# Performance work log

Hardware: AMD Instinct MI355X
Metric: run time of the kernel (lower is better)

The kernel has to match this reference:

```python
import jax, jax.numpy as jnp
import numpy as np

N, D, H, HD, R, K, TM = 32768, 128, 2, 64, 2, 32, 2
E_EDGES, M_MOTIFS, NG = 262144, 131072, 32
EPS = 1e-5
BETA_MAX = 5.0
GRAD_CLIP = 1.0
STATE_CLIP = 10.0
DAMPING = 1.0

def _isp(x):
    # inverse softplus of init values (params stored pre-softplus)
    return float(np.log(np.expm1(x)))

LAM2_RAW, LAM3_RAW, LAMM_RAW = _isp(1.0), _isp(0.5), _isp(1.0)
B2_RAW, B3_RAW, BM_RAW = _isp(1.0), _isp(1.0), _isp(1.0)


def layernorm(x, g, b):
    mu = x.mean(-1, keepdims=True)
    v = ((x - mu) ** 2).mean(-1, keepdims=True)
    return g * (x - mu) * jax.lax.rsqrt(v + EPS) + b


def seg_lse(s, seg, n, beta):
    # tempered logsumexp over segments: (1/beta) log sum_j exp(beta*s_j); s:[items,H] -> [n,H]
    sb = beta * s
    m = jax.ops.segment_max(sb, seg, num_segments=n)
    m = jnp.where(jnp.isfinite(m), m, 0.0)
    z = jax.ops.segment_sum(jnp.exp(sb - m[seg]), seg, num_segments=n)
    return jnp.where(z > 0, (m + jnp.log(jnp.maximum(z, 1e-30))) / beta, 0.0)


def energy(X, a_2, ln_gamma, ln_beta, W_Q2, W_K2, W_Q3, W_K3, T_tau, W_Qm, W_Km, B_mem,
           c_2, u_2, c_3, u_3, v_3, t_tau, batch):
    sp = jax.nn.softplus
    lam2, lam3, lamm = sp(LAM2_RAW), sp(LAM3_RAW), sp(LAMM_RAW)
    b2 = jnp.minimum(sp(B2_RAW), BETA_MAX)
    b3 = jnp.minimum(sp(B3_RAW), BETA_MAX)
    bm = jnp.minimum(sp(BM_RAW), BETA_MAX)
    G = layernorm(X, ln_gamma, ln_beta)
    # pairwise Q2/K2 term over edges (c_2 <- u_2) with learned per-edge bias a_2
    Q2 = jnp.einsum('nd,hzd->nhz', G, W_Q2)  # [N,H,HD]
    K2 = jnp.einsum('nd,hzd->nhz', G, W_K2)
    s2 = jnp.einsum('ehz,ehz->eh', Q2[c_2], K2[u_2]) / np.sqrt(HD) + a_2  # [E,H]
    e_pair = -lam2 * seg_lse(s2, c_2, N, b2).sum(-1)  # [N]
    # rank-R bilinear motif term over (c_3,u_3,v_3) with type embedding T_tau
    Q3 = jnp.einsum('nd,hzd->nhz', G, W_Q3).reshape(N, H, R, HD)
    K3 = jnp.einsum('nd,hzd->nhz', G, W_K3).reshape(N, H, R, HD)
    qk = jnp.einsum('mhrz,mhrz->mhr', Q3[c_3], K3[u_3])
    tv = jnp.einsum('mhrz,mhrz->mhr', T_tau[t_tau], K3[v_3])
    s3 = (qk * tv).sum(-1) / HD  # [M,H]
    e_motif = -lam3 * seg_lse(s3, c_3, N, b3).sum(-1)
    # K-slot memory term
    Qm = jnp.einsum('nd,hzd->nhz', G, W_Qm)
    Km = jnp.einsum('kd,hzd->hkz', B_mem, W_Km)
    sm = jnp.einsum('nhz,hkz->nhk', Qm, Km) / np.sqrt(HD)
    e_mem = -(lamm / bm) * jax.nn.logsumexp(bm * sm, axis=-1).sum(-1)
    e_node = 0.5 * (X * X).sum(-1) + e_pair + e_motif + e_mem
    return jax.ops.segment_sum(e_node, batch, num_segments=NG)  # per-graph energy [NG]


def setup_inputs() -> dict:
    key = jax.random.key(0)
    ks = jax.random.split(key, 16)
    inp = {}
    inp['X'] = jax.random.normal(ks[0], (N, D), jnp.float32)
    inp['c_2'] = jax.random.randint(ks[1], (E_EDGES,), 0, N)
    inp['u_2'] = jax.random.randint(ks[2], (E_EDGES,), 0, N)
    inp['c_3'] = jax.random.randint(ks[3], (M_MOTIFS,), 0, N)
    inp['u_3'] = jax.random.randint(ks[4], (M_MOTIFS,), 0, N)
    inp['v_3'] = jax.random.randint(ks[5], (M_MOTIFS,), 0, N)
    inp['t_tau'] = jax.random.randint(ks[6], (M_MOTIFS,), 0, TM)
    inp['batch'] = jnp.sort(jax.random.randint(ks[7], (N,), 0, NG))
    inp['a_2'] = 0.1 * jax.random.normal(ks[8], (E_EDGES, H), jnp.float32)
    inp['step_size'] = jnp.full((1,), 0.1, jnp.float32)
    inp['ln_gamma'] = jnp.ones((D,), jnp.float32)
    inp['ln_beta'] = jnp.zeros((D,), jnp.float32)
    s = 1.0 / np.sqrt(D)
    inp['W_Q2'] = s * jax.random.normal(ks[9], (H, HD, D), jnp.float32)
    inp['W_K2'] = s * jax.random.normal(ks[10], (H, HD, D), jnp.float32)
    inp['W_Q3'] = 0.5 * s * jax.random.normal(ks[11], (H, R * HD, D), jnp.float32)
    inp['W_K3'] = 0.5 * s * jax.random.normal(ks[12], (H, R * HD, D), jnp.float32)
    inp['T_tau'] = 0.02 * jax.random.normal(ks[13], (TM, H, R, HD), jnp.float32)
    inp['W_Qm'] = 0.5 * s * jax.random.normal(ks[14], (H, HD, D), jnp.float32)
    inp['W_Km'] = 0.5 * s * jax.random.normal(ks[15], (H, HD, D), jnp.float32)
    inp['B_mem'] = s * jax.random.normal(jax.random.fold_in(key, 99), (K, D), jnp.float32)
    return inp


def reference(X, c_2, u_2, c_3, u_3, v_3, t_tau, batch, a_2, step_size,
              ln_gamma, ln_beta, W_Q2, W_K2, W_Q3, W_K3, T_tau, W_Qm, W_Km, B_mem):
    Eg, vjp = jax.vjp(
        lambda Xv: energy(Xv, a_2, ln_gamma, ln_beta, W_Q2, W_K2, W_Q3, W_K3, T_tau,
                          W_Qm, W_Km, B_mem, c_2, u_2, c_3, u_3, v_3, t_tau, batch), X)
    gX, = vjp(jnp.ones_like(Eg))
    gnorm = jnp.linalg.norm(gX, axis=-1, keepdims=True)
    gX = gX * (GRAD_CLIP / jnp.maximum(gnorm, GRAD_CLIP))
    X_next = X - step_size[0] * DAMPING * gX
    snorm = jnp.linalg.norm(X_next, axis=-1, keepdims=True)
    X_next = X_next * (STATE_CLIP / jnp.maximum(snorm, STATE_CLIP))
    return X_next, Eg
```

## Files before the change

kernel.cpp:

```cpp
#include <hip/hip_runtime.h>
#include <hip/hip_bf16.h>
#include <math.h>

typedef __hip_bfloat16 bf16;
typedef short bf16x8 __attribute__((ext_vector_type(8)));
typedef float f32x4 __attribute__((ext_vector_type(4)));

#define N_NODES 32768
#define D_DIM 128
#define E_EDG 262144
#define M_MOT 131072
#define NG_G 32
#define F_TOT 832

__device__ __forceinline__ int pidx(int n){ return ((n & 7) << 12) | (n >> 3); }

__device__ __forceinline__ float wsum64(float v){
#pragma unroll
  for (int o = 32; o > 0; o >>= 1) v += __shfl_xor(v, o, 64);
  return v;
}
__device__ __forceinline__ float hsum32(float v){
#pragma unroll
  for (int o = 16; o > 0; o >>= 1) v += __shfl_xor(v, o, 64);
  return v;
}
__device__ __forceinline__ float hmax32(float v){
#pragma unroll
  for (int o = 16; o > 0; o >>= 1) v = fmaxf(v, __shfl_xor(v, o, 64));
  return v;
}
__device__ __forceinline__ float hsum8(float v){
#pragma unroll
  for (int o = 4; o > 0; o >>= 1) v += __shfl_xor(v, o, 64);
  return v;
}
__device__ __forceinline__ float bflo(unsigned u){ return __uint_as_float(u << 16); }
__device__ __forceinline__ float bfhi(unsigned u){ return __uint_as_float(u & 0xffff0000u); }
__device__ __forceinline__ unsigned packbf(float x, float y){
  bf16 a = __float2bfloat16(x), b = __float2bfloat16(y);
  unsigned short ua = *(unsigned short*)&a, ub = *(unsigned short*)&b;
  return (unsigned)ua | ((unsigned)ub << 16);
}
__device__ __forceinline__ void unpk8(uint4 p, float* f){
  f[0] = bflo(p.x); f[1] = bfhi(p.x); f[2] = bflo(p.y); f[3] = bfhi(p.y);
  f[4] = bflo(p.z); f[5] = bfhi(p.z); f[6] = bflo(p.w); f[7] = bfhi(p.w);
}

__global__ __launch_bounds__(256) void k_phaseA(
    const int* c2, const int* u2, const int* c3, const int* u3, const int* v3,
    const float* wq2, const float* wk2, const float* wq3, const float* wk3,
    const float* wqm, const float* wkm, const float* bmem, const float* Ttau,
    int* cnt, float* Wcat, bf16* Ttb, float* Mprod){
  __shared__ float KmL[64];
  int b = blockIdx.x, t = threadIdx.x;
  if (b < 1024){
    int* base = cnt + (size_t)(b & 7) * 5 * N_NODES;
    int i = b * 256 + t;
    atomicAdd(&base[pidx(c2[i])], 1);
    atomicAdd(&base[N_NODES + pidx(u2[i])], 1);
    if (i < M_MOT){
      atomicAdd(&base[2 * N_NODES + pidx(c3[i])], 1);
      atomicAdd(&base[3 * N_NODES + pidx(u3[i])], 1);
      atomicAdd(&base[4 * N_NODES + pidx(v3[i])], 1);
    }
  } else if (b < 1440){
    int idx = (b - 1024) * 256 + t;
    if (idx < 768 * D_DIM){
      int f = idx / D_DIM, d = idx - f * D_DIM;
      const float* src; int fr;
      if      (f < 128){ src = wq2; fr = f; }
      else if (f < 256){ src = wk2; fr = f - 128; }
      else if (f < 512){ src = wq3; fr = f - 256; }
      else             { src = wk3; fr = f - 512; }
      Wcat[f * D_DIM + d] = src[fr * D_DIM + d];
    } else {
      int j = idx - 768 * D_DIM;
      Ttb[j] = __float2bfloat16(Ttau[j]);
    }
  } else {
    int hk = b - 1440;
    int h = hk >> 5, k = hk & 31;
    if (t < 64){
      const float* wrow = wkm + (size_t)(h * 64 + t) * D_DIM;
      const float* brow = bmem + k * D_DIM;
      float acc = 0.f;
      for (int d = 0; d < D_DIM; d++) acc += wrow[d] * brow[d];
      KmL[t] = acc;
    }
    __syncthreads();
    if (t < 128){
      const float* w = wqm + (size_t)(h * 64) * 128 + t;
      float acc = 0.f;
      for (int z = 0; z < 64; z++) acc += w[z * 128] * KmL[z];
      Mprod[t * 64 + hk] = acc;
    }
  }
}

__global__ __launch_bounds__(1024) void k_phaseB(
    int* cntcur, int* off,
    const float* X, const float* gamma, const float* beta,
    bf16* Gb, float* mu, float* rstd, float* e_node,
    const float* Wcat, const float* Mprod, bf16* wfF, bf16* wfB){
  __shared__ int sd[1024];
  int b = blockIdx.x, t = threadIdx.x;
  if (b < 5){
    int a = b;
    int* cbase = cntcur + a * N_NODES;
    int* o = off + a * (N_NODES + 1);
    int loc[32];
    int sum = 0;
#pragma unroll
    for (int j = 0; j < 32; j++){
      int idx = t * 32 + j;
      int tot = 0;
#pragma unroll
      for (int rr = 0; rr < 8; rr++) tot += cbase[(size_t)rr * 5 * N_NODES + idx];
      loc[j] = sum; sum += tot;
    }
    sd[t] = sum;
    __syncthreads();
    for (int s = 1; s < 1024; s <<= 1){
      int v = (t >= s) ? sd[t - s] : 0;
      __syncthreads();
      sd[t] += v;
      __syncthreads();
    }
    int excl = sd[t] - sum;
#pragma unroll
    for (int j = 0; j < 32; j++){
      int val = excl + loc[j];
      o[t * 32 + j] = val;
      cbase[t * 32 + j] = val;
    }
    if (t == 1023) o[N_NODES] = sd[1023];
  } else if (b < 2053){
    int wv = t >> 6, l = t & 63;
    int n = (b - 5) * 16 + wv;
    float2 x2 = ((const float2*)(X + (size_t)n * 128))[l];
    float sumx = wsum64(x2.x + x2.y);
    float sumxx = wsum64(x2.x * x2.x + x2.y * x2.y);
    float m = sumx * (1.0f / 128.0f);
    float var = sumxx * (1.0f / 128.0f) - m * m;
    float rs = rsqrtf(var + 1e-5f);
    float2 gg = ((const float2*)gamma)[l];
    float2 bb = ((const float2*)beta)[l];
    ((unsigned*)(Gb + (size_t)n * 128))[l] =
        packbf(gg.x * (x2.x - m) * rs + bb.x, gg.y * (x2.y - m) * rs + bb.y);
    if (l == 0){ mu[n] = m; rstd[n] = rs; e_node[n] = 0.5f * sumxx; }
  } else {
    int idx = (b - 2053) * 1024 + t;
    int j = idx & 7, lane = (idx >> 3) & 63, tt = idx >> 9;
    {
      int tn = tt >> 2, kt = tt & 3;
      int f = tn * 16 + (lane & 15), d = kt * 32 + (lane >> 4) * 8 + j;
      float v = (f < 768) ? Wcat[f * 128 + d] : 0.125f * Mprod[d * 64 + (f - 768)];
      wfF[idx] = __float2bfloat16(v);
    }
    {
      int td = tt / 26, tf = tt - td * 26;
      int f = tf * 32 + (lane >> 4) * 8 + j, d = td * 16 + (lane & 15);
      float v = (f < 768) ? Wcat[f * 128 + d] : -0.125f * Mprod[d * 64 + (f - 768)];
      wfB[idx] = __float2bfloat16(v);
    }
  }
}

__global__ __launch_bounds__(256) void k_phaseC(
    const bf16* Gb, const bf16* wfF, bf16* P,
    const int* c2, const int* u2, const int* c3, const int* u3, const int* v3,
    const int* t3, int* cur,
    uint2* lec, uint2* leu, uint2* lmc, uint2* lmu, uint2* lmv){
  int b = blockIdx.x;
  int g = b / 29, r = b - g * 29;
  if (r < 13){
    __shared__ unsigned shP[64 * 36];
    int f = g * 13 + r;
    int bx = f & 511, by = f >> 9;
    int wave = threadIdx.x >> 6, lane = threadIdx.x & 63;
    int m0 = bx * 64 + wave * 16;
    int tn0 = by * 4;
    int rw = lane & 15, quad = lane >> 4;
    const bf16* aptr = Gb + (size_t)(m0 + rw) * 128 + quad * 8;
    bf16x8 a[4];
#pragma unroll
    for (int kt = 0; kt < 4; kt++) a[kt] = *(const bf16x8*)(aptr + kt * 32);
    f32x4 acc[4];
#pragma unroll
    for (int i = 0; i < 4; i++) acc[i] = (f32x4){0.f, 0.f, 0.f, 0.f};
#pragma unroll
    for (int nf = 0; nf < 4; nf++){
      int tn = tn0 + nf;
#pragma unroll
      for (int kt = 0; kt < 4; kt++){
        bf16x8 bb = *(const bf16x8*)(wfF + (((size_t)tn * 4 + kt) * 64 + lane) * 8);
        acc[nf] = __builtin_amdgcn_mfma_f32_16x16x32_bf16(bb, a[kt], acc[nf], 0, 0, 0);
      }
    }
    int lrow = wave * 16 + rw;
#pragma unroll
    for (int nf = 0; nf < 4; nf++){
      unsigned lo = packbf(acc[nf][0], acc[nf][1]);
      unsigned hi = packbf(acc[nf][2], acc[nf][3]);
      *(uint2*)&shP[lrow * 36 + nf * 8 + quad * 2] = make_uint2(lo, hi);
    }
    __syncthreads();
    int t = threadIdx.x;
    int orow = t >> 2, s = t & 3;
    uint4 v0 = *(const uint4*)&shP[orow * 36 + s * 4];
    uint4 v1 = *(const uint4*)&shP[orow * 36 + 16 + s * 4];
    uint4* prow = (uint4*)(P + (size_t)(bx * 64 + orow) * F_TOT) + tn0 * 2 + s;
    prow[0] = v0;
    prow[4] = v1;
  } else {
    int j = g * 16 + (r - 13);
    int range = j >> 3;
    int res = b & 7;
    int i = range * 256 + threadIdx.x;
    {
      int c = c2[i], u = u2[i];
      if ((c & 7) == res){
        int pos = atomicAdd(&cur[pidx(c)], 1);
        lec[pos] = make_uint2((unsigned)u, (unsigned)i);
      }
      if ((u & 7) == res){
        int pos = atomicAdd(&cur[N_NODES + pidx(u)], 1);
        leu[pos] = make_uint2((unsigned)c, (unsigned)i);
      }
    }
    if (i < M_MOT){
      int c = c3[i], u = u3[i], v = v3[i], mt = t3[i];
      if ((c & 7) == res){
        int pos = atomicAdd(&cur[2 * N_NODES + pidx(c)], 1);
        lmc[pos] = make_uint2((unsigned)(u | (v << 16)), (unsigned)(mt | (i << 5)));
      }
      if ((u & 7) == res){
        int pos = atomicAdd(&cur[3 * N_NODES + pidx(u)], 1);
        lmu[pos] = make_uint2((unsigned)c, (unsigned)i);
      }
      if ((v & 7) == res){
        int pos = atomicAdd(&cur[4 * N_NODES + pidx(v)], 1);
        lmv[pos] = make_uint2((unsigned)(c | (mt << 16)), (unsigned)i);
      }
    }
  }
}

__global__ __launch_bounds__(256) void k_fused_c(const bf16* P, const uint2* lec, const uint2* lmc,
                   const bf16* Ttb, const float* a2, const int* off_ec, const int* off_mc,
                   float* s2, float* rz2, float* s3, float* qkb, float* tvb, float* rz3,
                   bf16* dP, float* e_pair, float* e_mot, float* e_mem){
  int b = blockIdx.x;
  int type = b % 3, grp = b / 3;
  int wave = threadIdx.x >> 6, z = threadIdx.x & 63;
  int n = grp * 4 + wave;
  int l = z & 31, lh = z >> 5;
  int pn = pidx(n);

  if (type == 0){
    int q = z >> 4, l16 = z & 15, hg = l16 >> 3;
    int beg = off_ec[pn], end = off_ec[pn + 1];
    uint4 qp = ((const uint4*)(P + (size_t)n * F_TOT))[l16];
    float qv[8]; unpk8(qp, qv);
    float acc[8] = {0,0,0,0,0,0,0,0};
    float zz = 0.f;
    int iters = (end - beg + 3) >> 2;
    for (int it = 0; it < iters; it++){
      int idx = beg + 4 * it + q;
      bool valid = idx < end;
      int idc = valid ? idx : end - 1;
      uint2 pl = lec[idc];
      float2 av = *(const float2*)(a2 + (size_t)pl.y * 2);
      uint4 kp = ((const uint4*)(P + (size_t)pl.x * F_TOT + 128))[l16];
      float kv[8]; unpk8(kp, kv);
      float d = 0.f;
#pragma unroll
      for (int j = 0; j < 8; j++) d += qv[j] * kv[j];
      float s = hsum8(d) * 0.125f + (hg ? av.y : av.x);
      if (valid && (l16 & 7) == 0) s2[2 * pl.y + hg] = s;
      float ex = valid ? expf(s) : 0.f;
#pragma unroll
      for (int j = 0; j < 8; j++) acc[j] += ex * kv[j];
      zz += ex;
    }
#pragma unroll
    for (int j = 0; j < 8; j++){
      acc[j] += __shfl_xor(acc[j], 16, 64);
      acc[j] += __shfl_xor(acc[j], 32, 64);
    }
    zz += __shfl_xor(zz, 16, 64);
    zz += __shfl_xor(zz, 32, 64);
    float rz = (zz > 0.f) ? 1.0f / zz : 0.f;
    float coef = -0.125f * rz;
    if (z < 16){
      uint4 o;
      o.x = packbf(coef * acc[0], coef * acc[1]);
      o.y = packbf(coef * acc[2], coef * acc[3]);
      o.z = packbf(coef * acc[4], coef * acc[5]);
      o.w = packbf(coef * acc[6], coef * acc[7]);
      ((uint4*)(dP + (size_t)n * F_TOT))[l16] = o;
      if ((l16 & 7) == 0) rz2[n * 2 + hg] = rz;
    }
    float eterm = (zz > 0.f) ? -logf(zz) : 0.f;
    float eo = __shfl(eterm, 8, 64);
    if (z == 0) e_pair[n] = eterm + eo;
  } else if (type == 1){
    int g = l >> 3, hg = g >> 1;
    int beg = off_mc[pn], end = off_mc[pn + 1];
    uint4 qp = ((const uint4*)(P + (size_t)n * F_TOT + 256))[l];
    float qv[8]; unpk8(qp, qv);
    float acc[8] = {0,0,0,0,0,0,0,0};
    float zz = 0.f;
    int iters = (end - beg + 1) >> 1;
    for (int it = 0; it < iters; it++){
      int idx = beg + 2 * it + lh;
      bool valid = idx < end;
      int idc = valid ? idx : end - 1;
      uint2 pl = lmc[idc];
      int u = pl.x & 0xffff, v = pl.x >> 16;
      int tix = pl.y & 31; unsigned m = pl.y >> 5;
      uint4 kup = ((const uint4*)(P + (size_t)u * F_TOT + 512))[l];
      uint4 kvp = ((const uint4*)(P + (size_t)v * F_TOT + 512))[l];
      uint4 tp  = ((const uint4*)(Ttb + (size_t)tix * 256))[l];
      float k[8], vv[8], pt[8];
      unpk8(kup, k); unpk8(kvp, vv); unpk8(tp, pt);
      float dq = 0.f, dt = 0.f;
#pragma unroll
      for (int j = 0; j < 8; j++){ dq += qv[j] * k[j]; dt += pt[j] * vv[j]; }
      float qk = hsum8(dq);
      float tv = hsum8(dt);
      if (valid && (l & 7) == 0){ qkb[(size_t)4 * m + g] = qk; tvb[(size_t)4 * m + g] = tv; }
      float w = qk * tv;
      float s = (w + __shfl_xor(w, 8, 64)) * (1.0f / 64.0f);
      if (valid && (l & 15) == 0) s3[2 * m + hg] = s;
      float ex = valid ? expf(s) : 0.f;
      float et = ex * tv;
#pragma unroll
      for (int j = 0; j < 8; j++) acc[j] += et * k[j];
      zz += ex;
    }
#pragma unroll
    for (int j = 0; j < 8; j++) acc[j] += __shfl_xor(acc[j], 32, 64);
    zz += __shfl_xor(zz, 32, 64);
    float rz = (zz > 0.f) ? 1.0f / zz : 0.f;
    float coef = (-0.5f / 64.0f) * rz;
    if (z < 32){
      uint4 o;
      o.x = packbf(coef * acc[0], coef * acc[1]);
      o.y = packbf(coef * acc[2], coef * acc[3]);
      o.z = packbf(coef * acc[4], coef * acc[5]);
      o.w = packbf(coef * acc[6], coef * acc[7]);
      ((uint4*)(dP + (size_t)n * F_TOT + 256))[l] = o;
      if ((l & 15) == 0) rz3[n * 2 + hg] = rz;
    }
    float eterm = (zz > 0.f) ? -0.5f * logf(zz) : 0.f;
    float eo = __shfl(eterm, 16, 64);
    if (z == 0) e_mot[n] = eterm + eo;
  } else {
    unsigned short us = ((const unsigned short*)(P + (size_t)n * F_TOT + 768))[z];
    float s = __uint_as_float((unsigned)us << 16);
    float mx = hmax32(s);
    float ex = expf(s - mx);
    float se = hsum32(ex);
    float p = ex / se;
    bf16 pb = __float2bfloat16(p);
    ((unsigned short*)(dP + (size_t)n * F_TOT + 768))[z] = *(unsigned short*)&pb;
    float eterm = -(mx + logf(se));
    float eo = __shfl(eterm, z ^ 32, 64);
    if (z == 0) e_mem[n] = eterm + eo;
  }
}

__global__ __launch_bounds__(256) void k_phaseE(const bf16* P, const uint2* leu,
                    const uint2* lmu, const uint2* lmv, const bf16* Ttb,
                    const float* s2, const float* rz2, const float* s3, const float* rz3,
                    const float* qkb, const float* tvb,
                    const int* off_eu, const int* off_mu, const int* off_mv, bf16* dP,
                    const float* e_node, const float* e_pair, const float* e_mot,
                    const float* e_mem, const int* batch, float* Eg){
  __shared__ float eg[NG_G];
  int b = blockIdx.x;
  if (b < 128){
    int t = threadIdx.x;
    if (t < NG_G) eg[t] = 0.f;
    __syncthreads();
    int n = b * 256 + t;
    float e = e_node[n] + e_pair[n] + e_mot[n] + e_mem[n];
    atomicAdd(&eg[batch[n]], e);
    __syncthreads();
    if (t < NG_G) atomicAdd(&Eg[t], eg[t]);
    return;
  }
  int b2 = b - 128;
  int type = b2 & 1, grp = b2 >> 1;
  int wave = threadIdx.x >> 6, z = threadIdx.x & 63;
  int n = grp * 4 + wave;
  int pn = pidx(n);

  if (type == 0){
    int e8 = z >> 3, l8 = z & 7;
    int beg = off_eu[pn], end = off_eu[pn + 1];
    float acc[16];
#pragma unroll
    for (int j = 0; j < 16; j++) acc[j] = 0.f;
    int iters = (end - beg + 7) >> 3;
    for (int it = 0; it < iters; it++){
      int idx = beg + 8 * it + e8;
      bool valid = idx < end;
      int idc = valid ? idx : end - 1;
      uint2 pl = leu[idc];
      const uint4* qrow = (const uint4*)(P + (size_t)pl.x * F_TOT);
      uint4 qp0 = qrow[l8];
      uint4 qp1 = qrow[l8 + 8];
      float2 sv = *(const float2*)(s2 + 2 * (size_t)pl.y);
      float2 rv = *(const float2*)(rz2 + 2 * (size_t)pl.x);
      float qv0[8], qv1[8];
      unpk8(qp0, qv0); unpk8(qp1, qv1);
      float p0 = valid ? expf(sv.x) * rv.x : 0.f;
      float p1 = valid ? expf(sv.y) * rv.y : 0.f;
#pragma unroll
      for (int j = 0; j < 8; j++){
        acc[j]     += p0 * qv0[j];
        acc[8 + j] += p1 * qv1[j];
      }
    }
#pragma unroll
    for (int j = 0; j < 16; j++){
      acc[j] += __shfl_xor(acc[j], 8, 64);
      acc[j] += __shfl_xor(acc[j], 16, 64);
      acc[j] += __shfl_xor(acc[j], 32, 64);
    }
    if (z < 8){
      uint4 o0, o1;
      o0.x = packbf(-0.125f * acc[0], -0.125f * acc[1]);
      o0.y = packbf(-0.125f * acc[2], -0.125f * acc[3]);
      o0.z = packbf(-0.125f * acc[4], -0.125f * acc[5]);
      o0.w = packbf(-0.125f * acc[6], -0.125f * acc[7]);
      o1.x = packbf(-0.125f * acc[8], -0.125f * acc[9]);
      o1.y = packbf(-0.125f * acc[10], -0.125f * acc[11]);
      o1.z = packbf(-0.125f * acc[12], -0.125f * acc[13]);
      o1.w = packbf(-0.125f * acc[14], -0.125f * acc[15]);
      uint4* dst = (uint4*)(dP + (size_t)n * F_TOT + 128);
      dst[z] = o0;
      dst[z + 8] = o1;
    }
  } else {
    int m4 = z >> 4, l16 = z & 15;
    int g0 = l16 >> 3;
    float acc[16];
#pragma unroll
    for (int j = 0; j < 16; j++) acc[j] = 0.f;
    {
      int beg = off_mu[pn], end = off_mu[pn + 1];
      int iters = (end - beg + 3) >> 2;
      for (int it = 0; it < iters; it++){
        int idx = beg + 4 * it + m4;
        bool valid = idx < end;
        int idc = valid ? idx : end - 1;
        uint2 pl = lmu[idc];
        const uint4* qrow = (const uint4*)(P + (size_t)pl.x * F_TOT + 256);
        uint4 qp0 = qrow[l16];
        uint4 qp1 = qrow[l16 + 16];
        float2 sv = *(const float2*)(s3 + 2 * (size_t)pl.y);
        float2 rv = *(const float2*)(rz3 + 2 * (size_t)pl.x);
        float4 tq = *(const float4*)(tvb + 4 * (size_t)pl.y);
        float t0 = g0 ? tq.y : tq.x;
        float t1 = g0 ? tq.w : tq.z;
        float qv0[8], qv1[8];
        unpk8(qp0, qv0); unpk8(qp1, qv1);
        float w0 = valid ? expf(sv.x) * rv.x * t0 : 0.f;
        float w1 = valid ? expf(sv.y) * rv.y * t1 : 0.f;
#pragma unroll
        for (int j = 0; j < 8; j++){
          acc[j]     += w0 * qv0[j];
          acc[8 + j] += w1 * qv1[j];
        }
      }
    }
    {
      int beg = off_mv[pn], end = off_mv[pn + 1];
      int iters = (end - beg + 3) >> 2;
      for (int it = 0; it < iters; it++){
        int idx = beg + 4 * it + m4;
        bool valid = idx < end;
        int idc = valid ? idx : end - 1;
        uint2 pl = lmv[idc];
        unsigned c = pl.x & 0xffff, tix = pl.x >> 16;
        const uint4* trow = (const uint4*)(Ttb + (size_t)tix * 256);
        uint4 tp0 = trow[l16];
        uint4 tp1 = trow[l16 + 16];
        float2 sv = *(const float2*)(s3 + 2 * (size_t)pl.y);
        float2 rv = *(const float2*)(rz3 + 2 * (size_t)c);
        float4 qq = *(const float4*)(qkb + 4 * (size_t)pl.y);
        float q0 = g0 ? qq.y : qq.x;
        float q1 = g0 ? qq.w : qq.z;
        float pt0[8], pt1[8];
        unpk8(tp0, pt0); unpk8(tp1, pt1);
        float w0 = valid ? expf(sv.x) * rv.x * q0 : 0.f;
        float w1 = valid ? expf(sv.y) * rv.y * q1 : 0.f;
#pragma unroll
        for (int j = 0; j < 8; j++){
          acc[j]     += w0 * pt0[j];
          acc[8 + j] += w1 * pt1[j];
        }
      }
    }
#pragma unroll
    for (int j = 0; j < 16; j++){
      acc[j] += __shfl_xor(acc[j], 16, 64);
      acc[j] += __shfl_xor(acc[j], 32, 64);
    }
    const float cst = -0.5f / 64.0f;
    if (z < 16){
      uint4 o0, o1;
      o0.x = packbf(cst * acc[0], cst * acc[1]);
      o0.y = packbf(cst * acc[2], cst * acc[3]);
      o0.z = packbf(cst * acc[4], cst * acc[5]);
      o0.w = packbf(cst * acc[6], cst * acc[7]);
      o1.x = packbf(cst * acc[8], cst * acc[9]);
      o1.y = packbf(cst * acc[10], cst * acc[11]);
      o1.z = packbf(cst * acc[12], cst * acc[13]);
      o1.w = packbf(cst * acc[14], cst * acc[15]);
      uint4* dst = (uint4*)(dP + (size_t)n * F_TOT + 512);
      dst[l16] = o0;
      dst[l16 + 16] = o1;
    }
  }
}

__global__ __launch_bounds__(256) void k_bwd_mfma(const bf16* dP, const bf16* wfB, float* dG){
  int wave = threadIdx.x >> 6, lane = threadIdx.x & 63;
  int m0 = blockIdx.x * 64 + wave * 16;
  int rw = lane & 15, quad = lane >> 4;
  const bf16* aptr = dP + (size_t)(m0 + rw) * F_TOT + quad * 8;
  f32x4 acc[8];
#pragma unroll
  for (int i = 0; i < 8; i++) acc[i] = (f32x4){0.f, 0.f, 0.f, 0.f};
  for (int kt = 0; kt < 26; kt++){
    bf16x8 a = *(const bf16x8*)(aptr + kt * 32);
#pragma unroll
    for (int td = 0; td < 8; td++){
      bf16x8 b = *(const bf16x8*)(wfB + (((size_t)td * 26 + kt) * 64 + lane) * 8);
      acc[td] = __builtin_amdgcn_mfma_f32_16x16x32_bf16(a, b, acc[td], 0, 0, 0);
    }
  }
#pragma unroll
  for (int td = 0; td < 8; td++){
    int col = td * 16 + rw;
#pragma unroll
    for (int r = 0; r < 4; r++){
      int row = m0 + quad * 4 + r;
      dG[(size_t)row * 128 + col] = acc[td][r];
    }
  }
}

__global__ __launch_bounds__(256) void k_finalize(const float* X, const float* dG, const float* gamma,
                    const float* mu, const float* rstd, const float* step_p,
                    const float* Eg, float* out){
  int wave = threadIdx.x >> 6, l = threadIdx.x & 63;
  int n = blockIdx.x * 4 + wave;
  float2 x2 = ((const float2*)(X + (size_t)n * 128))[l];
  float2 dg2 = ((const float2*)(dG + (size_t)n * 128))[l];
  float2 gg = ((const float2*)gamma)[l];
  float rs = rstd[n], m = mu[n];
  float xh0 = (x2.x - m) * rs, xh1 = (x2.y - m) * rs;
  float dxh0 = dg2.x * gg.x, dxh1 = dg2.y * gg.y;
  float s1 = wsum64(dxh0 + dxh1);
  float s2v = wsum64(dxh0 * xh0 + dxh1 * xh1);
  float g0 = x2.x + rs * (dxh0 - s1 * (1.0f / 128) - xh0 * (s2v * (1.0f / 128)));
  float g1 = x2.y + rs * (dxh1 - s1 * (1.0f / 128) - xh1 * (s2v * (1.0f / 128)));
  float gn = sqrtf(wsum64(g0 * g0 + g1 * g1));
  float gc = 1.0f / fmaxf(gn, 1.0f);
  g0 *= gc; g1 *= gc;
  float step = step_p[0];
  float xn0 = x2.x - step * g0, xn1 = x2.y - step * g1;
  float sn = sqrtf(wsum64(xn0 * xn0 + xn1 * xn1));
  float sc = 10.0f / fmaxf(sn, 10.0f);
  ((float2*)(out + (size_t)n * 128))[l] = make_float2(xn0 * sc, xn1 * sc);
  if (blockIdx.x == 0 && threadIdx.x < NG_G)
    out[(size_t)N_NODES * 128 + threadIdx.x] = Eg[threadIdx.x];
}

extern "C" void kernel_launch(void* const* d_in, const int* in_sizes, int n_in,
                              void* d_out, int out_size, void* d_ws, size_t ws_size,
                              hipStream_t stream) {
  const float* X     = (const float*)d_in[0];
  const int*  c_2    = (const int*) d_in[1];
  const int*  u_2    = (const int*) d_in[2];
  const int*  c_3    = (const int*) d_in[3];
  const int*  u_3    = (const int*) d_in[4];
  const int*  v_3    = (const int*) d_in[5];
  const int*  t_tau  = (const int*) d_in[6];
  const int*  batch  = (const int*) d_in[7];
  const float* a_2   = (const float*)d_in[8];
  const float* step_s= (const float*)d_in[9];
  const float* ln_g  = (const float*)d_in[10];
  const float* ln_b  = (const float*)d_in[11];
  const float* W_Q2  = (const float*)d_in[12];
  const float* W_K2  = (const float*)d_in[13];
  const float* W_Q3  = (const float*)d_in[14];
  const float* W_K3  = (const float*)d_in[15];
  const float* T_tau = (const float*)d_in[16];
  const float* W_Qm  = (const float*)d_in[17];
  const float* W_Km  = (const float*)d_in[18];
  const float* B_mem = (const float*)d_in[19];
  float* out = (float*)d_out;

  char* wb = (char*)d_ws;
  float* Wcat   = (float*)wb; wb += 768 * D_DIM * 4;
  float* Mprod  = (float*)wb; wb += 8192 * 4;
  float* mu     = (float*)wb; wb += N_NODES * 4;
  float* rstd   = (float*)wb; wb += N_NODES * 4;
  float* s2     = (float*)wb; wb += (size_t)E_EDG * 2 * 4;
  float* rz2    = (float*)wb; wb += N_NODES * 2 * 4;
  float* s3     = (float*)wb; wb += (size_t)M_MOT * 2 * 4;
  float* qkb    = (float*)wb; wb += (size_t)M_MOT * 4 * 4;
  float* tvb    = (float*)wb; wb += (size_t)M_MOT * 4 * 4;
  float* rz3    = (float*)wb; wb += N_NODES * 2 * 4;
  float* e_node = (float*)wb; wb += N_NODES * 4;
  float* e_pair = (float*)wb; wb += N_NODES * 4;
  float* e_mot  = (float*)wb; wb += N_NODES * 4;
  float* e_mem  = (float*)wb; wb += N_NODES * 4;
  float* Eg     = (float*)wb; wb += NG_G * 4;
  float* dG     = (float*)wb; wb += (size_t)N_NODES * D_DIM * 4;
  bf16* Gb      = (bf16*)wb;  wb += (size_t)N_NODES * D_DIM * 2;
  bf16* P       = (bf16*)wb;  wb += (size_t)N_NODES * F_TOT * 2;
  bf16* dP      = (bf16*)wb;  wb += (size_t)N_NODES * F_TOT * 2;
  bf16* wfF     = (bf16*)wb;  wb += 106496 * 2;
  bf16* wfB     = (bf16*)wb;  wb += 106496 * 2;
  bf16* Ttb     = (bf16*)wb;  wb += 8192 * 2;
  int* cntcur   = (int*)wb;   wb += 8 * 5 * N_NODES * 4;
  int* off      = (int*)wb;   wb += 5 * (N_NODES + 1) * 4;
  wb = (char*)(((size_t)wb + 15) & ~(size_t)15);
  uint2* lec    = (uint2*)wb; wb += (size_t)E_EDG * 8;
  uint2* leu    = (uint2*)wb; wb += (size_t)E_EDG * 8;
  uint2* lmc    = (uint2*)wb; wb += (size_t)M_MOT * 8;
  uint2* lmu    = (uint2*)wb; wb += (size_t)M_MOT * 8;
  uint2* lmv    = (uint2*)wb; wb += (size_t)M_MOT * 8;

  const int* off_ec = off;
  const int* off_eu = off + (N_NODES + 1);
  const int* off_mc = off + 2 * (N_NODES + 1);
  const int* off_mu = off + 3 * (N_NODES + 1);
  const int* off_mv = off + 4 * (N_NODES + 1);

  hipMemsetAsync(cntcur, 0, (size_t)8 * 5 * N_NODES * sizeof(int), stream);
  hipMemsetAsync(Eg, 0, NG_G * sizeof(float), stream);
  hipLaunchKernelGGL(k_phaseA, dim3(1504), dim3(256), 0, stream,
                     c_2, u_2, c_3, u_3, v_3, W_Q2, W_K2, W_Q3, W_K3,
                     W_Qm, W_Km, B_mem, T_tau, cntcur, Wcat, Ttb, Mprod);
  hipLaunchKernelGGL(k_phaseB, dim3(2157), dim3(1024), 0, stream,
                     cntcur, off, X, ln_g, ln_b, Gb, mu, rstd, e_node,
                     Wcat, Mprod, wfF, wfB);
  hipLaunchKernelGGL(k_phaseC, dim3(512 * 29), dim3(256), 0, stream,
                     Gb, wfF, P, c_2, u_2, c_3, u_3, v_3, t_tau, cntcur,
                     lec, leu, lmc, lmu, lmv);
  hipLaunchKernelGGL(k_fused_c, dim3(3 * (N_NODES / 4)), dim3(256), 0, stream,
                     P, lec, lmc, Ttb, a_2, off_ec, off_mc,
                     s2, rz2, s3, qkb, tvb, rz3, dP, e_pair, e_mot, e_mem);
  hipLaunchKernelGGL(k_phaseE, dim3(128 + 2 * (N_NODES / 4)), dim3(256), 0, stream,
                     P, leu, lmu, lmv, Ttb, s2, rz2, s3, rz3, qkb, tvb,
                     off_eu, off_mu, off_mv, dP,
                     e_node, e_pair, e_mot, e_mem, batch, Eg);
  hipLaunchKernelGGL(k_bwd_mfma, dim3(N_NODES / 64), dim3(256), 0, stream, dP, wfB, dG);
  hipLaunchKernelGGL(k_finalize, dim3(N_NODES / 4), dim3(256), 0, stream,
                     X, dG, ln_g, mu, rstd, step_s, Eg, out);
}
```

Before: 401.9 us.

## Parallelize count reduction in separate kernel; process more edges per wave in fused gather

Moves the summation of eight replicated per-node counters out of the five-block scan in phaseB into a new wide kernel, so the scan blocks only read one vectorized count array. In k_fused_c, the pair and motif loops now have each lane handle both heads (8 lanes per edge, 16 per motif), so each wave iteration covers twice as many edges/motifs with wider per-lane loads and fewer shuffles per item. This costs an extra kernel launch and more registers per thread in the fused kernel.

```diff
diff --git a/kernel.cpp b/kernel.cpp
--- a/kernel.cpp
+++ b/kernel.cpp
@@ -98,6 +98,18 @@
   }
 }
 
+__global__ __launch_bounds__(256) void k_reduce8(int* cnt){
+  int idx = blockIdx.x * 256 + threadIdx.x;
+  int4* base = (int4*)cnt;
+  int4 s = base[idx];
+#pragma unroll
+  for (int rr = 1; rr < 8; rr++){
+    int4 v = *(const int4*)(cnt + (size_t)rr * 5 * N_NODES + 4 * (size_t)idx);
+    s.x += v.x; s.y += v.y; s.z += v.z; s.w += v.w;
+  }
+  base[idx] = s;
+}
+
 __global__ __launch_bounds__(1024) void k_phaseB(
     int* cntcur, int* off,
     const float* X, const float* gamma, const float* beta,
@@ -106,19 +118,17 @@
   __shared__ int sd[1024];
   int b = blockIdx.x, t = threadIdx.x;
   if (b < 5){
-    int a = b;
-    int* cbase = cntcur + a * N_NODES;
-    int* o = off + a * (N_NODES + 1);
+    int* c = cntcur + b * N_NODES;
+    int* o = off + b * (N_NODES + 1);
+    int4 lv[8];
+    const int4* c4 = (const int4*)c;
+#pragma unroll
+    for (int j4 = 0; j4 < 8; j4++) lv[j4] = c4[t * 8 + j4];
+    int* lvp = (int*)lv;
     int loc[32];
     int sum = 0;
 #pragma unroll
-    for (int j = 0; j < 32; j++){
-      int idx = t * 32 + j;
-      int tot = 0;
-#pragma unroll
-      for (int rr = 0; rr < 8; rr++) tot += cbase[(size_t)rr * 5 * N_NODES + idx];
-      loc[j] = sum; sum += tot;
-    }
+    for (int j = 0; j < 32; j++){ loc[j] = sum; sum += lvp[j]; }
     sd[t] = sum;
     __syncthreads();
     for (int s = 1; s < 1024; s <<= 1){
@@ -132,7 +142,7 @@
     for (int j = 0; j < 32; j++){
       int val = excl + loc[j];
       o[t * 32 + j] = val;
-      cbase[t * 32 + j] = val;
+      c[t * 32 + j] = val;
     }
     if (t == 1023) o[N_NODES] = sd[1023];
   } else if (b < 2053){
@@ -255,108 +265,154 @@
   int type = b % 3, grp = b / 3;
   int wave = threadIdx.x >> 6, z = threadIdx.x & 63;
   int n = grp * 4 + wave;
-  int l = z & 31, lh = z >> 5;
   int pn = pidx(n);
 
   if (type == 0){
-    int q = z >> 4, l16 = z & 15, hg = l16 >> 3;
+    int e8 = z >> 3, l8 = z & 7;
     int beg = off_ec[pn], end = off_ec[pn + 1];
-    uint4 qp = ((const uint4*)(P + (size_t)n * F_TOT))[l16];
-    float qv[8]; unpk8(qp, qv);
-    float acc[8] = {0,0,0,0,0,0,0,0};
-    float zz = 0.f;
-    int iters = (end - beg + 3) >> 2;
+    const uint4* qrow = (const uint4*)(P + (size_t)n * F_TOT);
+    uint4 qp0 = qrow[l8], qp1 = qrow[l8 + 8];
+    float qv0[8], qv1[8]; unpk8(qp0, qv0); unpk8(qp1, qv1);
+    float acc0[8] = {0,0,0,0,0,0,0,0}, acc1[8] = {0,0,0,0,0,0,0,0};
+    float zz0 = 0.f, zz1 = 0.f;
+    int iters = (end - beg + 7) >> 3;
     for (int it = 0; it < iters; it++){
-      int idx = beg + 4 * it + q;
+      int idx = beg + 8 * it + e8;
       bool valid = idx < end;
       int idc = valid ? idx : end - 1;
       uint2 pl = lec[idc];
       float2 av = *(const float2*)(a2 + (size_t)pl.y * 2);
-      uint4 kp = ((const uint4*)(P + (size_t)pl.x * F_TOT + 128))[l16];
-      float kv[8]; unpk8(kp, kv);
-      float d = 0.f;
-#pragma unroll
-      for (int j = 0; j < 8; j++) d += qv[j] * kv[j];
-      float s = hsum8(d) * 0.125f + (hg ? av.y : av.x);
-      if (valid && (l16 & 7) == 0) s2[2 * pl.y + hg] = s;
-      float ex = valid ? expf(s) : 0.f;
-#pragma unroll
-      for (int j = 0; j < 8; j++) acc[j] += ex * kv[j];
-      zz += ex;
+      const uint4* krow = (const uint4*)(P + (size_t)pl.x * F_TOT + 128);
+      uint4 kp0 = krow[l8], kp1 = krow[l8 + 8];
+      float kv0[8], kv1[8]; unpk8(kp0, kv0); unpk8(kp1, kv1);
+      float d0 = 0.f, d1 = 0.f;
+#pragma unroll
+      for (int j = 0; j < 8; j++){ d0 += qv0[j] * kv0[j]; d1 += qv1[j] * kv1[j]; }
+      float s0 = hsum8(d0) * 0.125f + av.x;
+      float s1 = hsum8(d1) * 0.125f + av.y;
+      if (valid && l8 == 0) *(float2*)(s2 + 2 * (size_t)pl.y) = make_float2(s0, s1);
+      float ex0 = valid ? expf(s0) : 0.f;
+      float ex1 = valid ? expf(s1) : 0.f;
+#pragma unroll
+      for (int j = 0; j < 8; j++){ acc0[j] += ex0 * kv0[j]; acc1[j] += ex1 * kv1[j]; }
+      zz0 += ex0; zz1 += ex1;
     }
 #pragma unroll
     for (int j = 0; j < 8; j++){
-      acc[j] += __shfl_xor(acc[j], 16, 64);
-      acc[j] += __shfl_xor(acc[j], 32, 64);
-    }
-    zz += __shfl_xor(zz, 16, 64);
-    zz += __shfl_xor(zz, 32, 64);
-    float rz = (zz > 0.f) ? 1.0f / zz : 0.f;
-    float coef = -0.125f * rz;
-    if (z < 16){
-      uint4 o;
-      o.x = packbf(coef * acc[0], coef * acc[1]);
-      o.y = packbf(coef * acc[2], coef * acc[3]);
-      o.z = packbf(coef * acc[4], coef * acc[5]);
-      o.w = packbf(coef * acc[6], coef * acc[7]);
-      ((uint4*)(dP + (size_t)n * F_TOT))[l16] = o;
-      if ((l16 & 7) == 0) rz2[n * 2 + hg] = rz;
-    }
-    float eterm = (zz > 0.f) ? -logf(zz) : 0.f;
-    float eo = __shfl(eterm, 8, 64);
-    if (z == 0) e_pair[n] = eterm + eo;
+      acc0[j] += __shfl_xor(acc0[j], 8, 64);
+      acc0[j] += __shfl_xor(acc0[j], 16, 64);
+      acc0[j] += __shfl_xor(acc0[j], 32, 64);
+      acc1[j] += __shfl_xor(acc1[j], 8, 64);
+      acc1[j] += __shfl_xor(acc1[j], 16, 64);
+      acc1[j] += __shfl_xor(acc1[j], 32, 64);
+    }
+    zz0 += __shfl_xor(zz0, 8, 64); zz0 += __shfl_xor(zz0, 16, 64); zz0 += __shfl_xor(zz0, 32, 64);
+    zz1 += __shfl_xor(zz1, 8, 64); zz1 += __shfl_xor(zz1, 16, 64); zz1 += __shfl_xor(zz1, 32, 64);
+    float rz0 = (zz0 > 0.f) ? 1.0f / zz0 : 0.f;
+    float rz1 = (zz1 > 0.f) ? 1.0f / zz1 : 0.f;
+    float c0 = -0.125f * rz0, c1 = -0.125f * rz1;
+    if (z < 8){
+      uint4 o0, o1;
+      o0.x = packbf(c0 * acc0[0], c0 * acc0[1]);
+      o0.y = packbf(c0 * acc0[2], c0 * acc0[3]);
+      o0.z = packbf(c0 * acc0[4], c0 * acc0[5]);
+      o0.w = packbf(c0 * acc0[6], c0 * acc0[7]);
+      o1.x = packbf(c1 * acc1[0], c1 * acc1[1]);
+      o1.y = packbf(c1 * acc1[2], c1 * acc1[3]);
+      o1.z = packbf(c1 * acc1[4], c1 * acc1[5]);
+      o1.w = packbf(c1 * acc1[6], c1 * acc1[7]);
+      uint4* dst = (uint4*)(dP + (size_t)n * F_TOT);
+      dst[z] = o0;
+      dst[z + 8] = o1;
+    }
+    if (z == 0){
+      *(float2*)(rz2 + 2 * (size_t)n) = make_float2(rz0, rz1);
+      float e0 = (zz0 > 0.f) ? -logf(zz0) : 0.f;
+      float e1 = (zz1 > 0.f) ? -logf(zz1) : 0.f;
+      e_pair[n] = e0 + e1;
+    }
   } else if (type == 1){
-    int g = l >> 3, hg = g >> 1;
+    int m4 = z >> 4, l16 = z & 15;
+    int rr = l16 >> 3;
     int beg = off_mc[pn], end = off_mc[pn + 1];
-    uint4 qp = ((const uint4*)(P + (size_t)n * F_TOT + 256))[l];
-    float qv[8]; unpk8(qp, qv);
-    float acc[8] = {0,0,0,0,0,0,0,0};
-    float zz = 0.f;
-    int iters = (end - beg + 1) >> 1;
+    const uint4* qrow = (const uint4*)(P + (size_t)n * F_TOT + 256);
+    uint4 qp0 = qrow[l16], qp1 = qrow[l16 + 16];
+    float qv0[8], qv1[8]; unpk8(qp0, qv0); unpk8(qp1, qv1);
+    float acc0[8] = {0,0,0,0,0,0,0,0}, acc1[8] = {0,0,0,0,0,0,0,0};
+    float zz0 = 0.f, zz1 = 0.f;
+    int iters = (end - beg + 3) >> 2;
     for (int it = 0; it < iters; it++){
-      int idx = beg + 2 * it + lh;
+      int idx = beg + 4 * it + m4;
       bool valid = idx < end;
       int idc = valid ? idx : end - 1;
       uint2 pl = lmc[idc];
       int u = pl.x & 0xffff, v = pl.x >> 16;
       int tix = pl.y & 31; unsigned m = pl.y >> 5;
-      uint4 kup = ((const uint4*)(P + (size_t)u * F_TOT + 512))[l];
-      uint4 kvp = ((const uint4*)(P + (size_t)v * F_TOT + 512))[l];
-      uint4 tp  = ((const uint4*)(Ttb + (size_t)tix * 256))[l];
-      float k[8], vv[8], pt[8];
-      unpk8(kup, k); unpk8(kvp, vv); unpk8(tp, pt);
-      float dq = 0.f, dt = 0.f;
-#pragma unroll
-      for (int j = 0; j < 8; j++){ dq += qv[j] * k[j]; dt += pt[j] * vv[j]; }
-      float qk = hsum8(dq);
-      float tv = hsum8(dt);
-      if (valid && (l & 7) == 0){ qkb[(size_t)4 * m + g] = qk; tvb[(size_t)4 * m + g] = tv; }
-      float w = qk * tv;
-      float s = (w + __shfl_xor(w, 8, 64)) * (1.0f / 64.0f);
-      if (valid && (l & 15) == 0) s3[2 * m + hg] = s;
-      float ex = valid ? expf(s) : 0.f;
-      float et = ex * tv;
-#pragma unroll
-      for (int j = 0; j < 8; j++) acc[j] += et * k[j];
-      zz += ex;
-    }
-#pragma unroll
-    for (int j = 0; j < 8; j++) acc[j] += __shfl_xor(acc[j], 32, 64);
-    zz += __shfl_xor(zz, 32, 64);
-    float rz = (zz > 0.f) ? 1.0f / zz : 0.f;
-    float coef = (-0.5f / 64.0f) * rz;
-    if (z < 32){
-      uint4 o;
-      o.x = packbf(coef * acc[0], coef * acc[1]);
-      o.y = packbf(coef * acc[2], coef * acc[3]);
-      o.z = packbf(coef * acc[4], coef * acc[5]);
-      o.w = packbf(coef * acc[6], coef * acc[7]);
-      ((uint4*)(dP + (size_t)n * F_TOT + 256))[l] = o;
-      if ((l & 15) == 0) rz3[n * 2 + hg] = rz;
-    }
-    float eterm = (zz > 0.f) ? -0.5f * logf(zz) : 0.f;
-    float eo = __shfl(eterm, 16, 64);
-    if (z == 0) e_mot[n] = eterm + eo;
+      const uint4* kurow = (const uint4*)(P + (size_t)u * F_TOT + 512);
+      const uint4* kvrow = (const uint4*)(P + (size_t)v * F_TOT + 512);
+      const uint4* trow  = (const uint4*)(Ttb + (size_t)tix * 256);
+      uint4 ku0 = kurow[l16], ku1 = kurow[l16 + 16];
+      uint4 kw0 = kvrow[l16], kw1 = kvrow[l16 + 16];
+      uint4 tp0 = trow[l16],  tp1 = trow[l16 + 16];
+      float k0[8], k1[8], vv0[8], vv1[8], pt0[8], pt1[8];
+      unpk8(ku0, k0); unpk8(ku1, k1);
+      unpk8(kw0, vv0); unpk8(kw1, vv1);
+      unpk8(tp0, pt0); unpk8(tp1, pt1);
+      float dq0 = 0.f, dq1 = 0.f, dt0 = 0.f, dt1 = 0.f;
+#pragma unroll
+      for (int j = 0; j < 8; j++){
+        dq0 += qv0[j] * k0[j]; dq1 += qv1[j] * k1[j];
+        dt0 += pt0[j] * vv0[j]; dt1 += pt1[j] * vv1[j];
+      }
+      float qk0 = hsum8(dq0), qk1 = hsum8(dq1);
+      float tv0 = hsum8(dt0), tv1 = hsum8(dt1);
+      if (valid && (l16 & 7) == 0){
+        qkb[(size_t)4 * m + rr] = qk0; qkb[(size_t)4 * m + 2 + rr] = qk1;
+        tvb[(size_t)4 * m + rr] = tv0; tvb[(size_t)4 * m + 2 + rr] = tv1;
+      }
+      float w0 = qk0 * tv0, w1 = qk1 * tv1;
+      float s0 = (w0 + __shfl_xor(w0, 8, 64)) * (1.0f / 64.0f);
+      float s1 = (w1 + __shfl_xor(w1, 8, 64)) * (1.0f / 64.0f);
+      if (valid && l16 == 0) *(float2*)(s3 + 2 * (size_t)m) = make_float2(s0, s1);
+      float ex0 = valid ? expf(s0) : 0.f;
+      float ex1 = valid ? expf(s1) : 0.f;
+      float et0 = ex0 * tv0, et1 = ex1 * tv1;
+#pragma unroll
+      for (int j = 0; j < 8; j++){ acc0[j] += et0 * k0[j]; acc1[j] += et1 * k1[j]; }
+      zz0 += ex0; zz1 += ex1;
+    }
+#pragma unroll
+    for (int j = 0; j < 8; j++){
+      acc0[j] += __shfl_xor(acc0[j], 16, 64);
+      acc0[j] += __shfl_xor(acc0[j], 32, 64);
+      acc1[j] += __shfl_xor(acc1[j], 16, 64);
+      acc1[j] += __shfl_xor(acc1[j], 32, 64);
+    }
+    zz0 += __shfl_xor(zz0, 16, 64); zz0 += __shfl_xor(zz0, 32, 64);
+    zz1 += __shfl_xor(zz1, 16, 64); zz1 += __shfl_xor(zz1, 32, 64);
+    float rz0 = (zz0 > 0.f) ? 1.0f / zz0 : 0.f;
+    float rz1 = (zz1 > 0.f) ? 1.0f / zz1 : 0.f;
+    float c0 = (-0.5f / 64.0f) * rz0, c1 = (-0.5f / 64.0f) * rz1;
+    if (z < 16){
+      uint4 o0, o1;
+      o0.x = packbf(c0 * acc0[0], c0 * acc0[1]);
+      o0.y = packbf(c0 * acc0[2], c0 * acc0[3]);
+      o0.z = packbf(c0 * acc0[4], c0 * acc0[5]);
+      o0.w = packbf(c0 * acc0[6], c0 * acc0[7]);
+      o1.x = packbf(c1 * acc1[0], c1 * acc1[1]);
+      o1.y = packbf(c1 * acc1[2], c1 * acc1[3]);
+      o1.z = packbf(c1 * acc1[4], c1 * acc1[5]);
+      o1.w = packbf(c1 * acc1[6], c1 * acc1[7]);
+      uint4* dst = (uint4*)(dP + (size_t)n * F_TOT + 256);
+      dst[l16] = o0;
+      dst[l16 + 16] = o1;
+    }
+    if (z == 0){
+      *(float2*)(rz3 + 2 * (size_t)n) = make_float2(rz0, rz1);
+      float e0 = (zz0 > 0.f) ? -0.5f * logf(zz0) : 0.f;
+      float e1 = (zz1 > 0.f) ? -0.5f * logf(zz1) : 0.f;
+      e_mot[n] = e0 + e1;
+    }
   } else {
     unsigned short us = ((const unsigned short*)(P + (size_t)n * F_TOT + 768))[z];
     float s = __uint_as_float((unsigned)us << 16);
@@ -651,6 +707,7 @@
   hipLaunchKernelGGL(k_phaseA, dim3(1504), dim3(256), 0, stream,
                      c_2, u_2, c_3, u_3, v_3, W_Q2, W_K2, W_Q3, W_K3,
                      W_Qm, W_Km, B_mem, T_tau, cntcur, Wcat, Ttb, Mprod);
+  hipLaunchKernelGGL(k_reduce8, dim3(160), dim3(256), 0, stream, cntcur);
   hipLaunchKernelGGL(k_phaseB, dim3(2157), dim3(1024), 0, stream,
                      cntcur, off, X, ln_g, ln_b, Gb, mu, rstd, e_node,
                      Wcat, Mprod, wfF, wfB);
```

Measured after the change: 394.7 us. About the same (-1.8%).
